# Kernel tuning notes

Measured on AMD Instinct MI355X. Metric: run time of the kernel, lower is better.

## Reference

```python
import jax, jax.numpy as jnp
import numpy as np

EPS = 1e-8  # torch F.cosine_similarity default eps


def setup_inputs() -> dict:
    key = jax.random.key(0)
    k1, k2 = jax.random.split(key)
    xs_pad = jax.random.normal(k1, (8, 8192, 256), dtype=jnp.float32)   # [B, T, D]
    spk_emb = jax.random.normal(k2, (8, 200, 256), dtype=jnp.float32)   # [B, S, D]
    return {"xs_pad": xs_pad, "spk_emb": spk_emb}


def reference(xs_pad, spk_emb):
    # Pairwise cosine similarity: [B, T, S]
    # Equivalent to F.cosine_similarity(xs.unsqueeze(2), spk.unsqueeze(1), dim=-1)
    # = dot(x, y) / max(||x|| * ||y||, eps)
    dot = jnp.einsum("btd,bsd->bts", xs_pad, spk_emb)
    nx = jnp.linalg.norm(xs_pad, axis=-1)    # [B, T]
    ny = jnp.linalg.norm(spk_emb, axis=-1)   # [B, S]
    denom = jnp.maximum(nx[:, :, None] * ny[:, None, :], EPS)
    return dot / denom
```

## Files before the change

kernel.cpp:

```cpp
#include <hip/hip_runtime.h>
#include <math.h>

typedef __attribute__((ext_vector_type(8))) _Float16 f16x8;
typedef __attribute__((ext_vector_type(4))) float f32x4;

#define BT 8192
#define BS 200
#define SP 208
#define DD 256
#define NJ 13
#define NKB 8
#define NSLOT 26
#define SLOT_H 512
#define TOT_SLOTS (8 * NKB * NSLOT)
#define NORM_OFF ((size_t)TOT_SLOTS * SLOT_H)
#define WS_NEED (NORM_OFF * 2 + 8 * SP * 4)

__device__ __forceinline__ void gl_lds16(const _Float16* g, _Float16* l) {
    __builtin_amdgcn_global_load_lds(
        (const __attribute__((address_space(1))) unsigned int*)g,
        (__attribute__((address_space(3))) unsigned int*)l, 16, 0, 0);
}

__global__ __launch_bounds__(256, 4)
void spk_prep_kernel(const float* __restrict__ SPK, _Float16* __restrict__ wsH) {
    const int j = blockIdx.x;
    const int b = blockIdx.y;
    const int tid = threadIdx.x;
    const int w = tid >> 6;
    const int lane = tid & 63;
    const int lr = lane & 15;
    const int lg = lane >> 4;
    const int srow = j * 16 + lr;
    const float* __restrict__ spk_b = SPK + (size_t)b * BS * DD;

    __shared__ float pn[4][16];
    float ss = 0.f;

    #pragma unroll
    for (int t = 0; t < 2; ++t) {
        int kb = w + t * 4;
        f16x8 hi, lo;
        if (srow < BS) {
            const float* src = spk_b + srow * DD + kb * 32 + lg * 8;
            float4 v0 = *(const float4*)src;
            float4 v1 = *(const float4*)(src + 4);
            float xv[8] = {v0.x, v0.y, v0.z, v0.w, v1.x, v1.y, v1.z, v1.w};
            #pragma unroll
            for (int e = 0; e < 8; ++e) {
                _Float16 h = (_Float16)xv[e];
                hi[e] = h;
                lo[e] = (_Float16)(xv[e] - (float)h);
                ss = fmaf(xv[e], xv[e], ss);
            }
        } else {
            #pragma unroll
            for (int e = 0; e < 8; ++e) { hi[e] = (_Float16)0.f; lo[e] = (_Float16)0.f; }
        }
        size_t base = ((size_t)(b * NKB + kb) * NSLOT + j) * SLOT_H + lane * 8;
        *(f16x8*)&wsH[base] = hi;
        *(f16x8*)&wsH[base + 13 * SLOT_H] = lo;
    }

    ss += __shfl_xor(ss, 16, 64);
    ss += __shfl_xor(ss, 32, 64);
    if (lane < 16) pn[w][lane] = ss;
    __syncthreads();
    if (tid < 16) {
        float s = pn[0][tid] + pn[1][tid] + pn[2][tid] + pn[3][tid];
        float* sn = (float*)(wsH + NORM_OFF);
        sn[b * SP + j * 16 + tid] = sqrtf(s);
    }
}

__global__ __launch_bounds__(512, 4)
void cos_main_kernel(const float* __restrict__ X, const _Float16* __restrict__ wsH,
                     float* __restrict__ OUT) {
    const int b   = blockIdx.y;
    const int t0  = blockIdx.x * 128;
    const int tid = threadIdx.x;
    const int wid = tid >> 6;
    const int lane = tid & 63;
    const int lr = lane & 15;
    const int lg = lane >> 4;

    __shared__ _Float16 Bb[2][NSLOT * SLOT_H];

    const float* __restrict__ xrow = X + ((size_t)b * BT + t0 + wid * 16 + lr) * DD;
    const float* __restrict__ snW = (const float*)(wsH + NORM_OFF) + b * SP;
    const _Float16* __restrict__ wsB = wsH + (size_t)b * NKB * NSLOT * SLOT_H;

    float4 pa0 = *(const float4*)(xrow + lg * 8);
    float4 pa1 = *(const float4*)(xrow + lg * 8 + 4);

    for (int s = wid; s < NSLOT; s += 8)
        gl_lds16(wsB + (size_t)s * SLOT_H + lane * 8, &Bb[0][s * SLOT_H]);
    __syncthreads();

    f32x4 acc[NJ];
    #pragma unroll
    for (int j = 0; j < NJ; ++j) acc[j] = (f32x4){0.f, 0.f, 0.f, 0.f};

    float ss = 0.f;
    int cur = 0;

    for (int kb = 0; kb < NKB; ++kb) {
        if (kb < NKB - 1) {
            const _Float16* src = wsB + (size_t)(kb + 1) * NSLOT * SLOT_H;
            for (int s = wid; s < NSLOT; s += 8)
                gl_lds16(src + (size_t)s * SLOT_H + lane * 8, &Bb[cur ^ 1][s * SLOT_H]);
            __builtin_amdgcn_sched_barrier(0);
        }

        f16x8 ahi, alo;
        {
            float xv[8] = {pa0.x, pa0.y, pa0.z, pa0.w, pa1.x, pa1.y, pa1.z, pa1.w};
            #pragma unroll
            for (int e = 0; e < 8; ++e) {
                _Float16 h = (_Float16)xv[e];
                ahi[e] = h;
                alo[e] = (_Float16)(xv[e] - (float)h);
                ss = fmaf(xv[e], xv[e], ss);
            }
        }
        if (kb < NKB - 1) {
            int o = (kb + 1) * 32 + lg * 8;
            pa0 = *(const float4*)(xrow + o);
            pa1 = *(const float4*)(xrow + o + 4);
        }

        const _Float16* __restrict__ bc = &Bb[cur][lane * 8];
        #pragma unroll
        for (int j = 0; j < NJ; ++j) {
            f16x8 bhi = *(const f16x8*)(bc + j * SLOT_H);
            f16x8 blo = *(const f16x8*)(bc + (13 + j) * SLOT_H);
            __builtin_amdgcn_s_setprio(1);
            acc[j] = __builtin_amdgcn_mfma_f32_16x16x32_f16(ahi, bhi, acc[j], 0, 0, 0);
            acc[j] = __builtin_amdgcn_mfma_f32_16x16x32_f16(alo, bhi, acc[j], 0, 0, 0);
            acc[j] = __builtin_amdgcn_mfma_f32_16x16x32_f16(ahi, blo, acc[j], 0, 0, 0);
            __builtin_amdgcn_s_setprio(0);
        }

        if (kb < NKB - 1) {
            asm volatile("s_waitcnt vmcnt(2)" ::: "memory");
            __builtin_amdgcn_s_barrier();
            __builtin_amdgcn_sched_barrier(0);
            cur ^= 1;
        }
    }

    ss += __shfl_xor(ss, 16, 64);
    ss += __shfl_xor(ss, 32, 64);

    #pragma unroll
    for (int reg = 0; reg < 4; ++reg) {
        int rc = lg * 4 + reg;
        float xn = sqrtf(__shfl(ss, rc, 64));
        int row = t0 + wid * 16 + rc;
        float* orow = OUT + ((size_t)b * BT + row) * BS;
        #pragma unroll
        for (int j = 0; j < NJ; ++j) {
            int col = j * 16 + lr;
            if (col < BS) {
                float denom = fmaxf(xn * snW[col], 1e-8f);
                orow[col] = acc[j][reg] * __builtin_amdgcn_rcpf(denom);
            }
        }
    }
}

#define TM 128
#define LSTR 40

__global__ __launch_bounds__(256, 2)
void cos_scorer_kernel(const float* __restrict__ X, const float* __restrict__ SPK,
                       float* __restrict__ OUT) {
    const int b   = blockIdx.y;
    const int t0  = blockIdx.x * TM;
    const int tid = threadIdx.x;
    const int wid = tid >> 6;
    const int lane = tid & 63;
    const int lr  = lane & 15;
    const int lg  = lane >> 4;

    __shared__ _Float16 Shi[SP * LSTR];
    __shared__ _Float16 Slo[SP * LSTR];
    __shared__ float sn_l[SP];

    const float* __restrict__ spk_b = SPK + (size_t)b * BS * DD;
    const float* __restrict__ xrow0 = X + ((size_t)b * BT + t0 + wid * 32 + lr) * DD;
    const float* __restrict__ xrow1 = xrow0 + 16 * DD;

    float4 pa00 = *(const float4*)(xrow0 + lg * 8);
    float4 pa01 = *(const float4*)(xrow0 + lg * 8 + 4);
    float4 pa10 = *(const float4*)(xrow1 + lg * 8);
    float4 pa11 = *(const float4*)(xrow1 + lg * 8 + 4);

    if (tid < SP) {
        float ss = 0.f;
        if (tid < BS) {
            const float4* p = (const float4*)(spk_b + tid * DD);
            #pragma unroll 8
            for (int i = 0; i < DD / 4; ++i) {
                float4 v = p[i];
                ss = fmaf(v.x, v.x, ss); ss = fmaf(v.y, v.y, ss);
                ss = fmaf(v.z, v.z, ss); ss = fmaf(v.w, v.w, ss);
            }
        }
        sn_l[tid] = sqrtf(ss);
    }

    f32x4 acc[2][NJ];
    #pragma unroll
    for (int rt = 0; rt < 2; ++rt)
        #pragma unroll
        for (int j = 0; j < NJ; ++j)
            acc[rt][j] = (f32x4){0.f, 0.f, 0.f, 0.f};

    float ss0 = 0.f, ss1 = 0.f;

    for (int kb = 0; kb < 8; ++kb) {
        for (int i = tid; i < SP * 4; i += 256) {
            int s = i >> 2, part = i & 3;
            f16x8 hi, lo;
            #pragma unroll
            for (int e = 0; e < 8; ++e) { hi[e] = (_Float16)0.f; lo[e] = (_Float16)0.f; }
            if (s < BS) {
                const float* src = spk_b + s * DD + kb * 32 + part * 8;
                float4 v0 = *(const float4*)src;
                float4 v1 = *(const float4*)(src + 4);
                float xv[8] = {v0.x, v0.y, v0.z, v0.w, v1.x, v1.y, v1.z, v1.w};
                #pragma unroll
                for (int e = 0; e < 8; ++e) {
                    _Float16 h = (_Float16)xv[e];
                    hi[e] = h;
                    lo[e] = (_Float16)(xv[e] - (float)h);
                }
            }
            int off = s * LSTR + part * 8;
            *(f16x8*)&Shi[off] = hi;
            *(f16x8*)&Slo[off] = lo;
        }
        __syncthreads();

        f16x8 ahi0, alo0, ahi1, alo1;
        {
            float xv0[8] = {pa00.x, pa00.y, pa00.z, pa00.w, pa01.x, pa01.y, pa01.z, pa01.w};
            float xv1[8] = {pa10.x, pa10.y, pa10.z, pa10.w, pa11.x, pa11.y, pa11.z, pa11.w};
            #pragma unroll
            for (int e = 0; e < 8; ++e) {
                _Float16 h0 = (_Float16)xv0[e];
                ahi0[e] = h0; alo0[e] = (_Float16)(xv0[e] - (float)h0);
                ss0 = fmaf(xv0[e], xv0[e], ss0);
                _Float16 h1 = (_Float16)xv1[e];
                ahi1[e] = h1; alo1[e] = (_Float16)(xv1[e] - (float)h1);
                ss1 = fmaf(xv1[e], xv1[e], ss1);
            }
        }
        if (kb < 7) {
            int o = (kb + 1) * 32 + lg * 8;
            pa00 = *(const float4*)(xrow0 + o);
            pa01 = *(const float4*)(xrow0 + o + 4);
            pa10 = *(const float4*)(xrow1 + o);
            pa11 = *(const float4*)(xrow1 + o + 4);
        }

        #pragma unroll
        for (int j = 0; j < NJ; ++j) {
            int boff = (j * 16 + lr) * LSTR + lg * 8;
            f16x8 bhi = *(const f16x8*)&Shi[boff];
            f16x8 blo = *(const f16x8*)&Slo[boff];
            acc[0][j] = __builtin_amdgcn_mfma_f32_16x16x32_f16(ahi0, bhi, acc[0][j], 0, 0, 0);
            acc[1][j] = __builtin_amdgcn_mfma_f32_16x16x32_f16(ahi1, bhi, acc[1][j], 0, 0, 0);
            acc[0][j] = __builtin_amdgcn_mfma_f32_16x16x32_f16(alo0, bhi, acc[0][j], 0, 0, 0);
            acc[1][j] = __builtin_amdgcn_mfma_f32_16x16x32_f16(alo1, bhi, acc[1][j], 0, 0, 0);
            acc[0][j] = __builtin_amdgcn_mfma_f32_16x16x32_f16(ahi0, blo, acc[0][j], 0, 0, 0);
            acc[1][j] = __builtin_amdgcn_mfma_f32_16x16x32_f16(ahi1, blo, acc[1][j], 0, 0, 0);
        }
        __syncthreads();
    }

    ss0 += __shfl_xor(ss0, 16, 64);
    ss0 += __shfl_xor(ss0, 32, 64);
    ss1 += __shfl_xor(ss1, 16, 64);
    ss1 += __shfl_xor(ss1, 32, 64);

    #pragma unroll
    for (int rt = 0; rt < 2; ++rt) {
        float ssv = rt ? ss1 : ss0;
        #pragma unroll
        for (int reg = 0; reg < 4; ++reg) {
            int rc = lg * 4 + reg;
            float xn = sqrtf(__shfl(ssv, rc, 64));
            int row = t0 + wid * 32 + rt * 16 + rc;
            float* orow = OUT + ((size_t)b * BT + row) * BS;
            #pragma unroll
            for (int j = 0; j < NJ; ++j) {
                int col = j * 16 + lr;
                if (col < BS) {
                    float denom = fmaxf(xn * sn_l[col], 1e-8f);
                    orow[col] = acc[rt][j][reg] * __builtin_amdgcn_rcpf(denom);
                }
            }
        }
    }
}

extern "C" void kernel_launch(void* const* d_in, const int* in_sizes, int n_in,
                              void* d_out, int out_size, void* d_ws, size_t ws_size,
                              hipStream_t stream) {
    const float* X   = (const float*)d_in[0];
    const float* SPK = (const float*)d_in[1];
    float* OUT = (float*)d_out;

    if (ws_size >= (size_t)WS_NEED) {
        _Float16* wsH = (_Float16*)d_ws;
        hipLaunchKernelGGL(spk_prep_kernel, dim3(NJ, 8), dim3(256), 0, stream, SPK, wsH);
        hipLaunchKernelGGL(cos_main_kernel, dim3(BT / 128, 8), dim3(512), 0, stream,
                           X, wsH, OUT);
    } else {
        hipLaunchKernelGGL(cos_scorer_kernel, dim3(BT / TM, 8), dim3(256), 0, stream,
                           X, SPK, OUT);
    }
}
```

Before: 123.3 us.

## Shrink main-kernel blocks, stagger K-block order, split MFMA accumulators

```diff
diff --git a/kernel.cpp b/kernel.cpp
--- a/kernel.cpp
+++ b/kernel.cpp
@@ -73,16 +73,17 @@
     }
 }
 
-__global__ __launch_bounds__(512, 4)
+__global__ __launch_bounds__(256, 3)
 void cos_main_kernel(const float* __restrict__ X, const _Float16* __restrict__ wsH,
                      float* __restrict__ OUT) {
     const int b   = blockIdx.y;
-    const int t0  = blockIdx.x * 128;
+    const int t0  = blockIdx.x * 64;
     const int tid = threadIdx.x;
     const int wid = tid >> 6;
     const int lane = tid & 63;
     const int lr = lane & 15;
     const int lg = lane >> 4;
+    const int phase = blockIdx.x & 3;
 
     __shared__ _Float16 Bb[2][NSLOT * SLOT_H];
 
@@ -90,24 +91,32 @@
     const float* __restrict__ snW = (const float*)(wsH + NORM_OFF) + b * SP;
     const _Float16* __restrict__ wsB = wsH + (size_t)b * NKB * NSLOT * SLOT_H;
 
-    float4 pa0 = *(const float4*)(xrow + lg * 8);
-    float4 pa1 = *(const float4*)(xrow + lg * 8 + 4);
-
-    for (int s = wid; s < NSLOT; s += 8)
-        gl_lds16(wsB + (size_t)s * SLOT_H + lane * 8, &Bb[0][s * SLOT_H]);
+    int kb0 = phase;
+    float4 pa0 = *(const float4*)(xrow + kb0 * 32 + lg * 8);
+    float4 pa1 = *(const float4*)(xrow + kb0 * 32 + lg * 8 + 4);
+
+    {
+        const _Float16* src = wsB + (size_t)kb0 * NSLOT * SLOT_H;
+        for (int s = wid; s < NSLOT; s += 4)
+            gl_lds16(src + (size_t)s * SLOT_H + lane * 8, &Bb[0][s * SLOT_H]);
+    }
     __syncthreads();
 
-    f32x4 acc[NJ];
-    #pragma unroll
-    for (int j = 0; j < NJ; ++j) acc[j] = (f32x4){0.f, 0.f, 0.f, 0.f};
+    f32x4 accA[NJ], accB[NJ];
+    #pragma unroll
+    for (int j = 0; j < NJ; ++j) {
+        accA[j] = (f32x4){0.f, 0.f, 0.f, 0.f};
+        accB[j] = (f32x4){0.f, 0.f, 0.f, 0.f};
+    }
 
     float ss = 0.f;
     int cur = 0;
 
-    for (int kb = 0; kb < NKB; ++kb) {
-        if (kb < NKB - 1) {
-            const _Float16* src = wsB + (size_t)(kb + 1) * NSLOT * SLOT_H;
-            for (int s = wid; s < NSLOT; s += 8)
+    for (int kbi = 0; kbi < NKB; ++kbi) {
+        if (kbi < NKB - 1) {
+            int nkb = (phase + kbi + 1) & 7;
+            const _Float16* src = wsB + (size_t)nkb * NSLOT * SLOT_H;
+            for (int s = wid; s < NSLOT; s += 4)
                 gl_lds16(src + (size_t)s * SLOT_H + lane * 8, &Bb[cur ^ 1][s * SLOT_H]);
             __builtin_amdgcn_sched_barrier(0);
         }
@@ -123,8 +132,8 @@
                 ss = fmaf(xv[e], xv[e], ss);
             }
         }
-        if (kb < NKB - 1) {
-            int o = (kb + 1) * 32 + lg * 8;
+        if (kbi < NKB - 1) {
+            int o = ((phase + kbi + 1) & 7) * 32 + lg * 8;
             pa0 = *(const float4*)(xrow + o);
             pa1 = *(const float4*)(xrow + o + 4);
         }
@@ -135,13 +144,13 @@
             f16x8 bhi = *(const f16x8*)(bc + j * SLOT_H);
             f16x8 blo = *(const f16x8*)(bc + (13 + j) * SLOT_H);
             __builtin_amdgcn_s_setprio(1);
-            acc[j] = __builtin_amdgcn_mfma_f32_16x16x32_f16(ahi, bhi, acc[j], 0, 0, 0);
-            acc[j] = __builtin_amdgcn_mfma_f32_16x16x32_f16(alo, bhi, acc[j], 0, 0, 0);
-            acc[j] = __builtin_amdgcn_mfma_f32_16x16x32_f16(ahi, blo, acc[j], 0, 0, 0);
+            accA[j] = __builtin_amdgcn_mfma_f32_16x16x32_f16(ahi, bhi, accA[j], 0, 0, 0);
+            accB[j] = __builtin_amdgcn_mfma_f32_16x16x32_f16(alo, bhi, accB[j], 0, 0, 0);
+            accB[j] = __builtin_amdgcn_mfma_f32_16x16x32_f16(ahi, blo, accB[j], 0, 0, 0);
             __builtin_amdgcn_s_setprio(0);
         }
 
-        if (kb < NKB - 1) {
+        if (kbi < NKB - 1) {
             asm volatile("s_waitcnt vmcnt(2)" ::: "memory");
             __builtin_amdgcn_s_barrier();
             __builtin_amdgcn_sched_barrier(0);
@@ -163,7 +172,7 @@
             int col = j * 16 + lr;
             if (col < BS) {
                 float denom = fmaxf(xn * snW[col], 1e-8f);
-                orow[col] = acc[j][reg] * __builtin_amdgcn_rcpf(denom);
+                orow[col] = (accA[j][reg] + accB[j][reg]) * __builtin_amdgcn_rcpf(denom);
             }
         }
     }
@@ -316,7 +325,7 @@
     if (ws_size >= (size_t)WS_NEED) {
         _Float16* wsH = (_Float16*)d_ws;
         hipLaunchKernelGGL(spk_prep_kernel, dim3(NJ, 8), dim3(256), 0, stream, SPK, wsH);
-        hipLaunchKernelGGL(cos_main_kernel, dim3(BT / 128, 8), dim3(512), 0, stream,
+        hipLaunchKernelGGL(cos_main_kernel, dim3(BT / 64, 8), dim3(256), 0, stream,
                            X, wsH, OUT);
     } else {
         hipLaunchKernelGGL(cos_scorer_kernel, dim3(BT / TM, 8), dim3(256), 0, stream,
```

After: 136.2 us. 1.1x slower.
